# Kernel optimization log

Measured on AMD Instinct MI355X. Metric: run time of the kernel, lower is better.

Reference implementation:

```python
import jax, jax.numpy as jnp
import numpy as np

NUM_PATCHES = 128  # static stand-in for max(patch_ids)+1


def setup_inputs() -> dict:
    key = jax.random.key(0)
    k1, k2, k3, k4 = jax.random.split(key, 4)
    B, S, H, D = 8, 8192, 512, 768
    byte_hiddens = jax.random.normal(k1, (B, S, H), dtype=jnp.float32)
    patch_ids = jnp.sort(jax.random.randint(k2, (B, S), 0, NUM_PATCHES), axis=-1)
    # Dense output_projection (glorot-uniform-ish init)
    lim = float(np.sqrt(6.0 / (H + D)))
    W_proj = jax.random.uniform(k3, (H, D), minval=-lim, maxval=lim, dtype=jnp.float32)
    b_proj = jnp.zeros((D,), dtype=jnp.float32)
    return {"byte_hiddens": byte_hiddens, "W_proj": W_proj, "b_proj": b_proj,
            "patch_ids": patch_ids}


def reference(byte_hiddens, W_proj, b_proj, patch_ids):
    # Mean pooling within patches: for each patch p, mean of byte_hiddens where
    # patch_ids == p (sum / max(count, 1)), then Dense projection.
    B, S, H = byte_hiddens.shape
    P = NUM_PATCHES
    # Flatten batch into segment ids so one segment_sum covers all (b, p) pairs.
    seg = (patch_ids + jnp.arange(B, dtype=patch_ids.dtype)[:, None] * P).reshape(-1)
    flat = byte_hiddens.reshape(B * S, H)
    sums = jax.ops.segment_sum(flat, seg, num_segments=B * P)          # [B*P, H]
    counts = jax.ops.segment_sum(jnp.ones((B * S,), byte_hiddens.dtype), seg,
                                 num_segments=B * P)                   # [B*P]
    means = sums / jnp.maximum(counts, 1.0)[:, None]                   # [B*P, H]
    means = means.reshape(B, P, H)
    return means @ W_proj + b_proj                                     # [B, P, D]
```

## Files before the change

### kernel.cpp

```cpp
#include <hip/hip_runtime.h>

#define B_ 8
#define S_ 8192
#define H_ 512
#define D_ 768
#define P_ 128

__global__ __launch_bounds__(256) void pool_kernel(
    const float* __restrict__ bh, const int* __restrict__ ids,
    float* __restrict__ means)
{
    const int p = blockIdx.x;
    const int b = blockIdx.y;
    const int t = threadIdx.x;
    const int* row = ids + (size_t)b * S_;

    int lo = 0, hi = S_;
    while (lo < hi) { int mid = (lo + hi) >> 1; if (row[mid] < p) lo = mid + 1; else hi = mid; }
    const int start = lo;
    hi = S_;
    while (lo < hi) { int mid = (lo + hi) >> 1; if (row[mid] <= p) lo = mid + 1; else hi = mid; }
    const int end = lo;
    const int cnt = end - start;

    const float2* src = (const float2*)(bh + ((size_t)b * S_ + (size_t)start) * H_) + t;
    float ax0 = 0.f, ay0 = 0.f, ax1 = 0.f, ay1 = 0.f;
    int r = 0;
    for (; r + 2 <= cnt; r += 2) {
        float2 v0 = src[(size_t)r * (H_ / 2)];
        float2 v1 = src[(size_t)(r + 1) * (H_ / 2)];
        ax0 += v0.x; ay0 += v0.y;
        ax1 += v1.x; ay1 += v1.y;
    }
    if (r < cnt) {
        float2 v = src[(size_t)r * (H_ / 2)];
        ax0 += v.x; ay0 += v.y;
    }
    const float inv = 1.0f / (float)(cnt > 0 ? cnt : 1);
    float2 o;
    o.x = (ax0 + ax1) * inv;
    o.y = (ay0 + ay1) * inv;
    ((float2*)(means + ((size_t)(b * P_ + p)) * H_))[t] = o;
}

__global__ __launch_bounds__(256) void gemm_kernel(
    const float* __restrict__ A, const float* __restrict__ W,
    const float* __restrict__ bias, float* __restrict__ C)
{
    const int K = H_, N = D_;
    __shared__ float As[16][68];
    __shared__ float Bs[16][64];

    const int t  = threadIdx.x;
    const int tx = t & 15;
    const int ty = t >> 4;
    const int m0 = blockIdx.y * 64;
    const int n0 = blockIdx.x * 64;

    float acc[4][4] = {};

    for (int k0 = 0; k0 < K; k0 += 16) {
        #pragma unroll
        for (int i = 0; i < 4; ++i) {
            int idx = t + i * 256;
            int m = idx >> 4, k = idx & 15;
            As[k][m] = A[(size_t)(m0 + m) * K + (k0 + k)];
        }
        #pragma unroll
        for (int i = 0; i < 4; ++i) {
            int idx = t + i * 256;
            int k = idx >> 6, n = idx & 63;
            Bs[k][n] = W[(size_t)(k0 + k) * N + (n0 + n)];
        }
        __syncthreads();

        #pragma unroll
        for (int k = 0; k < 16; ++k) {
            float4 a4 = *(const float4*)&As[k][ty * 4];
            float4 b4 = *(const float4*)&Bs[k][tx * 4];
            const float a[4] = {a4.x, a4.y, a4.z, a4.w};
            const float bb[4] = {b4.x, b4.y, b4.z, b4.w};
            #pragma unroll
            for (int i = 0; i < 4; ++i)
                #pragma unroll
                for (int j = 0; j < 4; ++j)
                    acc[i][j] += a[i] * bb[j];
        }
        __syncthreads();
    }

    #pragma unroll
    for (int i = 0; i < 4; ++i) {
        const int m = m0 + ty * 4 + i;
        #pragma unroll
        for (int j = 0; j < 4; ++j) {
            const int n = n0 + tx * 4 + j;
            C[(size_t)m * N + n] = acc[i][j] + bias[n];
        }
    }
}

extern "C" void kernel_launch(void* const* d_in, const int* in_sizes, int n_in,
                              void* d_out, int out_size, void* d_ws, size_t ws_size,
                              hipStream_t stream) {
    const float* bh   = (const float*)d_in[0];
    const float* W    = (const float*)d_in[1];
    const float* bias = (const float*)d_in[2];
    const int*   ids  = (const int*)d_in[3];
    float* out   = (float*)d_out;
    float* means = (float*)d_ws;

    dim3 g1(P_, B_);
    pool_kernel<<<g1, 256, 0, stream>>>(bh, ids, means);

    dim3 g2(D_ / 64, (B_ * P_) / 64);
    gemm_kernel<<<g2, 256, 0, stream>>>(means, W, bias, out);
}
```

Measured before the change: 239.4 us.

## Precompute segment bounds, vectorize pooling with float4 rows, prefetch GEMM tiles

A new small kernel computes each patch's start offset once per batch, which removes the two binary searches every pool block used to run. The pool kernel now reads float4 and splits the rows of each patch between two halves of the block, then combines them through shared memory. The GEMM loads its next K tile into registers while the current tile is being computed, and writes the output with float4 stores and a vectorized bias load. This adds one extra kernel launch and a bounds buffer in the workspace.

```diff
diff --git a/kernel.cpp b/kernel.cpp
--- a/kernel.cpp
+++ b/kernel.cpp
@@ -6,41 +6,62 @@
 #define D_ 768
 #define P_ 128
 
+__global__ __launch_bounds__(128) void bounds_kernel(
+    const int* __restrict__ ids, int* __restrict__ bounds)
+{
+    const int b = blockIdx.x;
+    const int p = threadIdx.x;
+    const int* row = ids + (size_t)b * S_;
+    int lo = 0, hi = S_;
+    #pragma unroll 13
+    while (lo < hi) { int mid = (lo + hi) >> 1; if (row[mid] < p) lo = mid + 1; else hi = mid; }
+    bounds[b * (P_ + 1) + p] = lo;
+    if (p == 0) bounds[b * (P_ + 1) + P_] = S_;
+}
+
 __global__ __launch_bounds__(256) void pool_kernel(
-    const float* __restrict__ bh, const int* __restrict__ ids,
+    const float* __restrict__ bh, const int* __restrict__ bounds,
     float* __restrict__ means)
 {
     const int p = blockIdx.x;
     const int b = blockIdx.y;
     const int t = threadIdx.x;
-    const int* row = ids + (size_t)b * S_;
+    const int c = t & 127;
+    const int r_ofs = t >> 7;
 
-    int lo = 0, hi = S_;
-    while (lo < hi) { int mid = (lo + hi) >> 1; if (row[mid] < p) lo = mid + 1; else hi = mid; }
-    const int start = lo;
-    hi = S_;
-    while (lo < hi) { int mid = (lo + hi) >> 1; if (row[mid] <= p) lo = mid + 1; else hi = mid; }
-    const int end = lo;
-    const int cnt = end - start;
+    const int start = bounds[b * (P_ + 1) + p];
+    const int end   = bounds[b * (P_ + 1) + p + 1];
+    const int cnt   = end - start;
 
-    const float2* src = (const float2*)(bh + ((size_t)b * S_ + (size_t)start) * H_) + t;
-    float ax0 = 0.f, ay0 = 0.f, ax1 = 0.f, ay1 = 0.f;
-    int r = 0;
-    for (; r + 2 <= cnt; r += 2) {
-        float2 v0 = src[(size_t)r * (H_ / 2)];
-        float2 v1 = src[(size_t)(r + 1) * (H_ / 2)];
-        ax0 += v0.x; ay0 += v0.y;
-        ax1 += v1.x; ay1 += v1.y;
+    const float4* src = (const float4*)(bh + ((size_t)b * S_ + (size_t)start) * H_) + c;
+    float4 a0 = {0.f, 0.f, 0.f, 0.f};
+    float4 a1 = {0.f, 0.f, 0.f, 0.f};
+
+    int r = r_ofs;
+    for (; r + 2 < cnt; r += 4) {
+        float4 v0 = src[(size_t)r * (H_ / 4)];
+        float4 v1 = src[(size_t)(r + 2) * (H_ / 4)];
+        a0.x += v0.x; a0.y += v0.y; a0.z += v0.z; a0.w += v0.w;
+        a1.x += v1.x; a1.y += v1.y; a1.z += v1.z; a1.w += v1.w;
     }
     if (r < cnt) {
-        float2 v = src[(size_t)r * (H_ / 2)];
-        ax0 += v.x; ay0 += v.y;
+        float4 v = src[(size_t)r * (H_ / 4)];
+        a0.x += v.x; a0.y += v.y; a0.z += v.z; a0.w += v.w;
     }
-    const float inv = 1.0f / (float)(cnt > 0 ? cnt : 1);
-    float2 o;
-    o.x = (ax0 + ax1) * inv;
-    o.y = (ay0 + ay1) * inv;
-    ((float2*)(means + ((size_t)(b * P_ + p)) * H_))[t] = o;
+    float4 s;
+    s.x = a0.x + a1.x; s.y = a0.y + a1.y; s.z = a0.z + a1.z; s.w = a0.w + a1.w;
+
+    __shared__ float4 red[128];
+    if (r_ofs == 1) red[c] = s;
+    __syncthreads();
+    if (r_ofs == 0) {
+        float4 o = red[c];
+        const float inv = 1.0f / (float)(cnt > 0 ? cnt : 1);
+        float4 out;
+        out.x = (s.x + o.x) * inv; out.y = (s.y + o.y) * inv;
+        out.z = (s.z + o.z) * inv; out.w = (s.w + o.w) * inv;
+        ((float4*)(means + ((size_t)(b * P_ + p)) * H_))[c] = out;
+    }
 }
 
 __global__ __launch_bounds__(256) void gemm_kernel(
@@ -57,22 +78,30 @@
     const int m0 = blockIdx.y * 64;
     const int n0 = blockIdx.x * 64;
 
+    const int am = t >> 2;
+    const int ak = (t & 3) * 4;
+    const int bk = t >> 4;
+    const int bn = (t & 15) * 4;
+    const float* Aptr = A + (size_t)(m0 + am) * K + ak;
+    const float* Wptr = W + (size_t)bk * N + (n0 + bn);
+
+    float4 a_reg = *(const float4*)Aptr;
+    float4 b_reg = *(const float4*)Wptr;
+
     float acc[4][4] = {};
 
     for (int k0 = 0; k0 < K; k0 += 16) {
-        #pragma unroll
-        for (int i = 0; i < 4; ++i) {
-            int idx = t + i * 256;
-            int m = idx >> 4, k = idx & 15;
-            As[k][m] = A[(size_t)(m0 + m) * K + (k0 + k)];
+        As[ak + 0][am] = a_reg.x;
+        As[ak + 1][am] = a_reg.y;
+        As[ak + 2][am] = a_reg.z;
+        As[ak + 3][am] = a_reg.w;
+        *(float4*)&Bs[bk][bn] = b_reg;
+        __syncthreads();
+
+        if (k0 + 16 < K) {
+            a_reg = *(const float4*)(Aptr + (k0 + 16));
+            b_reg = *(const float4*)(Wptr + (size_t)(k0 + 16) * N);
         }
-        #pragma unroll
-        for (int i = 0; i < 4; ++i) {
-            int idx = t + i * 256;
-            int k = idx >> 6, n = idx & 63;
-            Bs[k][n] = W[(size_t)(k0 + k) * N + (n0 + n)];
-        }
-        __syncthreads();
 
         #pragma unroll
         for (int k = 0; k < 16; ++k) {
@@ -89,14 +118,17 @@
         __syncthreads();
     }
 
+    const float4 bv = *(const float4*)&bias[n0 + tx * 4];
+    const float badd[4] = {bv.x, bv.y, bv.z, bv.w};
     #pragma unroll
     for (int i = 0; i < 4; ++i) {
         const int m = m0 + ty * 4 + i;
-        #pragma unroll
-        for (int j = 0; j < 4; ++j) {
-            const int n = n0 + tx * 4 + j;
-            C[(size_t)m * N + n] = acc[i][j] + bias[n];
-        }
+        float4 o;
+        o.x = acc[i][0] + badd[0];
+        o.y = acc[i][1] + badd[1];
+        o.z = acc[i][2] + badd[2];
+        o.w = acc[i][3] + badd[3];
+        *(float4*)&C[(size_t)m * N + n0 + tx * 4] = o;
     }
 }
 
@@ -109,9 +141,12 @@
     const int*   ids  = (const int*)d_in[3];
     float* out   = (float*)d_out;
     float* means = (float*)d_ws;
+    int*   bounds = (int*)(means + (size_t)B_ * P_ * H_);
+
+    bounds_kernel<<<dim3(B_), 128, 0, stream>>>(ids, bounds);
 
     dim3 g1(P_, B_);
-    pool_kernel<<<g1, 256, 0, stream>>>(bh, ids, means);
+    pool_kernel<<<g1, 256, 0, stream>>>(bh, bounds, means);
 
     dim3 g2(D_ / 64, (B_ * P_) / 64);
     gemm_kernel<<<g2, 256, 0, stream>>>(means, W, bias, out);
```

New measurement: 229.1 us. -4.3%, faster.
